# Kernel tuning notes

Measured on AMD Instinct MI355X. Metric: run time of the kernel, lower is better.

## Reference

```python
import jax, jax.numpy as jnp
import numpy as np

B, S, D = 2, 2048, 2048
H, DH, DC = 16, 128, 32  # heads, head dim, compressed dim


def setup_inputs() -> dict:
    key = jax.random.key(0)
    ks = jax.random.split(key, 9)
    sc = 0.02
    return {
        "hidden_states": jax.random.normal(ks[0], (B, S, D), jnp.float32),
        "Wq": jax.random.normal(ks[1], (D, D), jnp.float32) * sc,
        "Wk": jax.random.normal(ks[2], (D, D), jnp.float32) * sc,
        "Wv": jax.random.normal(ks[3], (D, D), jnp.float32) * sc,
        "Wo": jax.random.normal(ks[4], (D, D), jnp.float32) * sc,
        "Wkc": jax.random.normal(ks[5], (DH, DC), jnp.float32) * sc,
        "Wvc": jax.random.normal(ks[6], (DH, DC), jnp.float32) * sc,
        "Wke": jax.random.normal(ks[7], (DC, DH), jnp.float32) * sc,
        "Wve": jax.random.normal(ks[8], (DC, DH), jnp.float32) * sc,
    }


def reference(hidden_states, Wq, Wk, Wv, Wo, Wkc, Wvc, Wke, Wve):
    # Project to per-head Q/K/V: [B, H, S, DH]
    def proj(W):
        return jnp.einsum("bsd,de->bse", hidden_states, W).reshape(B, S, H, DH).transpose(0, 2, 1, 3)

    q = proj(Wq)
    k_full = proj(Wk)
    v_full = proj(Wv)

    # Compress K/V (low-rank down-projection, per head): [B, H, S, DC]
    k_compressed = jnp.einsum("bhsd,dc->bhsc", k_full, Wkc)
    v_compressed = jnp.einsum("bhsd,dc->bhsc", v_full, Wvc)

    # Expand compressed cache back to full head dim (expand_mode='pre')
    k_hat = jnp.einsum("bhsc,cd->bhsd", k_compressed, Wke)
    v_hat = jnp.einsum("bhsc,cd->bhsd", v_compressed, Wve)

    # Causal scaled-dot-product attention
    scale = 1.0 / jnp.sqrt(jnp.asarray(DH, jnp.float32))
    scores = jnp.einsum("bhqd,bhkd->bhqk", q, k_hat) * scale
    causal = jnp.tril(jnp.ones((S, S), bool))
    scores = jnp.where(causal[None, None], scores, jnp.finfo(scores.dtype).min)
    probs = jax.nn.softmax(scores, axis=-1)
    ctx = jnp.einsum("bhqk,bhkd->bhqd", probs, v_hat)  # [B, H, S, DH]

    attn_out = jnp.einsum("bsd,de->bse", ctx.transpose(0, 2, 1, 3).reshape(B, S, D), Wo)
    return attn_out, k_compressed, v_compressed
```

## Files before the change

### kernel.cpp

```cpp
#include <hip/hip_runtime.h>

using u16 = unsigned short;
using u32 = unsigned int;

typedef __attribute__((ext_vector_type(8))) __bf16 bf16x8;
typedef __attribute__((ext_vector_type(4))) float f32x4;
typedef __attribute__((ext_vector_type(4))) u32 u32x4;

#define GLOAD16(gp, lp) __builtin_amdgcn_global_load_lds( \
    (const __attribute__((address_space(1))) void*)(gp),  \
    (__attribute__((address_space(3))) void*)(lp), 16, 0, 0)

__device__ __forceinline__ u16 f2b(float f) {
  u32 u = __builtin_bit_cast(u32, f);
  u += 0x7fffu + ((u >> 16) & 1u);
  return (u16)(u >> 16);
}
__device__ __forceinline__ float b2f(u16 h) {
  return __builtin_bit_cast(float, (u32)h << 16);
}
__device__ __forceinline__ u32 cvtpk(float lo, float hi) {
  u32 r;
  asm("v_cvt_pk_bf16_f32 %0, %1, %2" : "=v"(r) : "v"(lo), "v"(hi));
  return r;
}

__global__ __launch_bounds__(256) void cast_k(
    const float* __restrict__ in, u16* __restrict__ o1, int n) {
  int i = (blockIdx.x * 256 + threadIdx.x) * 4;
  if (i >= n) return;
  float4 v = *(const float4*)&in[i];
  *(uint2*)&o1[i] = make_uint2((u32)f2b(v.x) | ((u32)f2b(v.y) << 16),
                               (u32)f2b(v.z) | ((u32)f2b(v.w) << 16));
}

__global__ __launch_bounds__(256) void transpose_cast_k(
    const float* __restrict__ in, u16* __restrict__ out, int D) {
  __shared__ float t[32][33];
  const int tx = threadIdx.x & 31, ty = threadIdx.x >> 5;
  const int e0 = blockIdx.x * 32, d0 = blockIdx.y * 32;
  #pragma unroll
  for (int i = ty; i < 32; i += 8) t[i][tx] = in[(size_t)(d0 + i) * D + e0 + tx];
  __syncthreads();
  #pragma unroll
  for (int i = ty; i < 32; i += 8) out[(size_t)(e0 + i) * D + d0 + tx] = f2b(t[tx][i]);
}

__global__ __launch_bounds__(256) void combine_k(
    const float* __restrict__ Wfull, const float* __restrict__ Wc,
    u16* __restrict__ outT, int D) {
  __shared__ float wl[4096];
  const int tid = threadIdx.x;
  for (int i = tid; i < 4096; i += 256) wl[i] = Wc[i];
  __syncthreads();
  const int h = blockIdx.y;
  const int d = blockIdx.x * 256 + tid;
  const float* wkr = Wfull + (size_t)d * D + h * 128;
  float acc[32] = {};
  for (int dp = 0; dp < 128; ++dp) {
    const float wv = wkr[dp];
    const float* w2 = &wl[dp * 32];
    #pragma unroll
    for (int c = 0; c < 32; ++c) acc[c] += wv * w2[c];
  }
  #pragma unroll
  for (int c = 0; c < 32; ++c)
    outT[(size_t)(h * 32 + c) * D + d] = f2b(acc[c]);
}

__global__ __launch_bounds__(256) void wtrans_k(
    const float* __restrict__ in, u16* __restrict__ out) {
  const int i = blockIdx.x * 256 + threadIdx.x;
  const int d = i >> 5, c = i & 31;
  out[i] = f2b(in[c * 128 + d]);
}

template <int TRANS>
__global__ __launch_bounds__(256) void expand_mfma_k(
    const u16* __restrict__ in, const u16* __restrict__ WT, u16* __restrict__ out) {
  __shared__ alignas(16) u16 WL[128 * 32];
  __shared__ alignas(16) u16 ct[64 * 40];
  const int tid = threadIdx.x, lane = tid & 63, w = tid >> 6;
  const int cl = lane & 15, g = lane >> 4;
  const int bh = blockIdx.y, s0 = blockIdx.x * 64;
  for (int i = tid; i < 512; i += 256) ((uint4*)WL)[i] = ((const uint4*)WT)[i];
  {
    const int r = tid >> 2, co = (tid & 3) * 8;
    *(uint4*)&ct[r * 40 + co] =
        *(const uint4*)&in[((size_t)bh * 2048 + s0 + r) * 32 + co];
  }
  __syncthreads();
  f32x4 acc[2][4] = {};
  #pragma unroll
  for (int dti = 0; dti < 2; ++dti) {
    const bf16x8 wf = *(const bf16x8*)&WL[((w * 2 + dti) * 16 + cl) * 32 + g * 8];
    #pragma unroll
    for (int st = 0; st < 4; ++st) {
      const bf16x8 cf = *(const bf16x8*)&ct[(st * 16 + cl) * 40 + g * 8];
      if constexpr (TRANS)
        acc[dti][st] = __builtin_amdgcn_mfma_f32_16x16x32_bf16(wf, cf, acc[dti][st], 0, 0, 0);
      else
        acc[dti][st] = __builtin_amdgcn_mfma_f32_16x16x32_bf16(cf, wf, acc[dti][st], 0, 0, 0);
    }
  }
  #pragma unroll
  for (int dti = 0; dti < 2; ++dti) {
    #pragma unroll
    for (int st = 0; st < 4; ++st) {
      #pragma unroll
      for (int r = 0; r < 4; ++r) {
        if constexpr (TRANS) {
          const int d = (w * 2 + dti) * 16 + g * 4 + r;
          const int s = s0 + st * 16 + cl;
          out[((size_t)bh * 128 + d) * 2048 + s] = f2b(acc[dti][st][r]);
        } else {
          const int s = s0 + st * 16 + g * 4 + r;
          const int d = (w * 2 + dti) * 16 + cl;
          out[((size_t)bh * 2048 + s) * 128 + d] = f2b(acc[dti][st][r]);
        }
      }
    }
  }
}

__global__ __launch_bounds__(256) void gemm_qkv_k(
    const u16* __restrict__ A, const u16* __restrict__ Bt,
    u16* __restrict__ qb, float* __restrict__ out_kc, u16* __restrict__ kcb,
    float* __restrict__ out_vc, u16* __restrict__ vcb) {
  __shared__ alignas(16) u16 As[128 * 64];
  __shared__ alignas(16) u16 Bs[128 * 64];
  const int tid = threadIdx.x, lane = tid & 63, w = tid >> 6;
  const int l15 = lane & 15, lhi = lane >> 4;
  const int m0 = blockIdx.y * 128, n0 = blockIdx.x * 128;
  const int wr = (w >> 1) * 64, wc = (w & 1) * 64;
  const int rl = lane >> 3, cbe = (lane & 7) * 8;
  const int K = 2048;

  f32x4 acc[4][4] = {};

  for (int k0 = 0; k0 < K; k0 += 64) {
    __syncthreads();
    #pragma unroll
    for (int i = 0; i < 4; ++i) {
      const int rb = w * 32 + i * 8;
      GLOAD16(A + (size_t)(m0 + rb + rl) * K + k0 + cbe, &As[rb * 64]);
      GLOAD16(Bt + (size_t)(n0 + rb + rl) * K + k0 + cbe, &Bs[rb * 64]);
    }
    __syncthreads();
    #pragma unroll
    for (int ks = 0; ks < 2; ++ks) {
      bf16x8 af[4], bfr[4];
      #pragma unroll
      for (int m = 0; m < 4; ++m)
        af[m] = *(const bf16x8*)&As[(wr + m * 16 + l15) * 64 + ks * 32 + lhi * 8];
      #pragma unroll
      for (int n = 0; n < 4; ++n)
        bfr[n] = *(const bf16x8*)&Bs[(wc + n * 16 + l15) * 64 + ks * 32 + lhi * 8];
      #pragma unroll
      for (int m = 0; m < 4; ++m)
        #pragma unroll
        for (int n = 0; n < 4; ++n)
          acc[m][n] = __builtin_amdgcn_mfma_f32_16x16x32_bf16(af[m], bfr[n], acc[m][n], 0, 0, 0);
    }
  }

  const float qscale = 0.08838834764831845f * 1.4426950408889634f;
  #pragma unroll
  for (int m = 0; m < 4; ++m) {
    #pragma unroll
    for (int n = 0; n < 4; ++n) {
      #pragma unroll
      for (int r = 0; r < 4; ++r) {
        const int row = m0 + wr + m * 16 + lhi * 4 + r;
        const int col = n0 + wc + n * 16 + l15;
        const int b = row >> 11, s = row & 2047;
        const float v = acc[m][n][r];
        if (n0 < 2048) {
          const int h = col >> 7, dh = col & 127;
          qb[((size_t)(b * 16 + h) * 2048 + s) * 128 + dh] = f2b(v * qscale);
        } else {
          const int cc = col - 2048;
          if (cc < 512) {
            const int h = cc >> 5, c = cc & 31;
            const size_t idx = ((size_t)(b * 16 + h) * 2048 + s) * 32 + c;
            out_kc[idx] = v;
            kcb[idx] = f2b(v);
          } else {
            const int cc2 = cc - 512;
            const int h = cc2 >> 5, c = cc2 & 31;
            const size_t idx = ((size_t)(b * 16 + h) * 2048 + s) * 32 + c;
            out_vc[idx] = v;
            vcb[idx] = f2b(v);
          }
        }
      }
    }
  }
}

__global__ __launch_bounds__(256) void gemm_o_k(
    const u16* __restrict__ A, const u16* __restrict__ Bt,
    int M, int N, int K, float* __restrict__ outF) {
  __shared__ alignas(16) u16 As[128 * 64];
  __shared__ alignas(16) u16 Bs[128 * 64];
  const int tid = threadIdx.x, lane = tid & 63, w = tid >> 6;
  const int l15 = lane & 15, lhi = lane >> 4;
  const int m0 = blockIdx.y * 128, n0 = blockIdx.x * 128;
  const int wr = (w >> 1) * 64, wc = (w & 1) * 64;
  const int rl = lane >> 3, cbe = (lane & 7) * 8;

  f32x4 acc[4][4] = {};

  for (int k0 = 0; k0 < K; k0 += 64) {
    __syncthreads();
    #pragma unroll
    for (int i = 0; i < 4; ++i) {
      const int rb = w * 32 + i * 8;
      GLOAD16(A + (size_t)(m0 + rb + rl) * K + k0 + cbe, &As[rb * 64]);
      GLOAD16(Bt + (size_t)(n0 + rb + rl) * K + k0 + cbe, &Bs[rb * 64]);
    }
    __syncthreads();
    #pragma unroll
    for (int ks = 0; ks < 2; ++ks) {
      bf16x8 af[4], bfr[4];
      #pragma unroll
      for (int m = 0; m < 4; ++m)
        af[m] = *(const bf16x8*)&As[(wr + m * 16 + l15) * 64 + ks * 32 + lhi * 8];
      #pragma unroll
      for (int n = 0; n < 4; ++n)
        bfr[n] = *(const bf16x8*)&Bs[(wc + n * 16 + l15) * 64 + ks * 32 + lhi * 8];
      #pragma unroll
      for (int m = 0; m < 4; ++m)
        #pragma unroll
        for (int n = 0; n < 4; ++n)
          acc[m][n] = __builtin_amdgcn_mfma_f32_16x16x32_bf16(af[m], bfr[n], acc[m][n], 0, 0, 0);
    }
  }

  #pragma unroll
  for (int m = 0; m < 4; ++m)
    #pragma unroll
    for (int n = 0; n < 4; ++n)
      #pragma unroll
      for (int r = 0; r < 4; ++r)
        outF[(size_t)(m0 + wr + m * 16 + lhi * 4 + r) * N + n0 + wc + n * 16 + l15] =
            acc[m][n][r];
}

__global__ __launch_bounds__(512, 4) void attn_k(
    const u16* __restrict__ q, const u16* __restrict__ kh,
    const u16* __restrict__ vt, u16* __restrict__ ctx) {
  __shared__ alignas(16) u16 Ks[2][64 * 128];
  __shared__ alignas(16) u16 Vs[2][128 * 64];
  const int tid = threadIdx.x, lane = tid & 63, w = tid >> 6;
  const int grp = w >> 2, wq = w & 3;
  const int c = lane & 15, g = lane >> 4;
  const int iA = blockIdx.x, iB = 31 - iA, bh = blockIdx.y;
  const int qt = grp ? iB : iA;
  const size_t base = (size_t)bh * (2048 * 128);

  bf16x8 qf[4];
  {
    const int qrow = qt * 64 + wq * 16 + c;
    #pragma unroll
    for (int ks = 0; ks < 4; ++ks)
      qf[ks] = *(const bf16x8*)&q[base + (size_t)qrow * 128 + ks * 32 + g * 8];
  }

  f32x4 of[8] = {};
  float m = -__builtin_inff(), l = 0.f;
  const int srcLo = lane ^ (((4 - g) & 3) << 4);
  const int srcHi = lane ^ (((g + 1) & 3) << 4);
  const int alS = (lane & 48) + ((lane & 48) >> 2);
  const bool hiSel = (g >> 1) != 0;

#define STAGE(J, BUF)                                                          \
  {                                                                            \
    _Pragma("unroll")                                                          \
    for (int i2 = 0; i2 < 2; ++i2) {                                           \
      const int rowgrp = w * 8 + i2 * 4;                                       \
      const int rloc = rowgrp + (lane >> 4);                                   \
      const int srce = ((c * 16) ^ ((rloc & 7) << 4)) >> 1;                    \
      GLOAD16(kh + base + (size_t)((J) * 64 + rloc) * 128 + srce,              \
              &Ks[BUF][rowgrp * 128]);                                         \
    }                                                                          \
    _Pragma("unroll")                                                          \
    for (int i2 = 0; i2 < 2; ++i2) {                                           \
      const int d0 = (w * 2 + i2) * 8;                                         \
      const int dd = d0 + (lane >> 3);                                         \
      const int cc = lane & 7;                                                 \
      GLOAD16(vt + base + (size_t)dd * 2048 + (J) * 64 + ((cc ^ (dd & 7)) * 8),\
              &Vs[BUF][d0 * 64]);                                              \
    }                                                                          \
  }

  STAGE(0, 0);
  for (int j = 0; j <= iB; ++j) {
    const int buf = j & 1;
    __syncthreads();
    if (j < iB) STAGE(j + 1, buf ^ 1);
    if (j <= qt) {
      f32x4 sf[4] = {};
      const char* ksb0 = (const char*)&Ks[buf][0];
      __builtin_amdgcn_s_setprio(1);
      #pragma unroll
      for (int n = 0; n < 4; ++n) {
        const int row = n * 16 + c;
        const char* kb = ksb0 + row * 256;
        #pragma unroll
        for (int ks = 0; ks < 4; ++ks) {
          const bf16x8 kf =
              *(const bf16x8*)(kb + ((ks * 64 + g * 16) ^ ((row & 7) << 4)));
          sf[n] = __builtin_amdgcn_mfma_f32_16x16x32_bf16(kf, qf[ks], sf[n], 0, 0, 0);
        }
      }
      __builtin_amdgcn_s_setprio(0);
      if (j == qt) {
        const int qloc = wq * 16 + c;
        #pragma unroll
        for (int n = 0; n < 4; ++n)
          #pragma unroll
          for (int r = 0; r < 4; ++r)
            if (n * 16 + g * 4 + r > qloc) sf[n][r] = -__builtin_inff();
      }
      float smax = sf[0][0];
      #pragma unroll
      for (int n = 0; n < 4; ++n)
        #pragma unroll
        for (int r = 0; r < 4; ++r) smax = fmaxf(smax, sf[n][r]);
      smax = fmaxf(smax, __shfl_xor(smax, 16, 64));
      smax = fmaxf(smax, __shfl_xor(smax, 32, 64));
      if (__any(smax - m > 12.0f)) {
        const float mn = fmaxf(m, smax);
        const float al = exp2f(m - mn);
        m = mn;
        l *= al;
        float alr[4];
        #pragma unroll
        for (int r = 0; r < 4; ++r) alr[r] = __shfl(al, alS + r, 64);
        #pragma unroll
        for (int nd = 0; nd < 8; ++nd)
          #pragma unroll
          for (int r = 0; r < 4; ++r) of[nd][r] *= alr[r];
      }
      float rs = 0.f;
      #pragma unroll
      for (int n = 0; n < 4; ++n)
        #pragma unroll
        for (int r = 0; r < 4; ++r) {
          const float p = exp2f(sf[n][r] - m);
          sf[n][r] = p;
          rs += p;
        }
      rs += __shfl_xor(rs, 16, 64);
      rs += __shfl_xor(rs, 32, 64);
      l += rs;
      u32 pk0[4], pk1[4];
      #pragma unroll
      for (int n = 0; n < 4; ++n) {
        pk0[n] = cvtpk(sf[n][0], sf[n][1]);
        pk1[n] = cvtpk(sf[n][2], sf[n][3]);
      }
      bf16x8 pf[2];
      #pragma unroll
      for (int ks2 = 0; ks2 < 2; ++ks2) {
        const int na = ks2 * 2, nb = ks2 * 2 + 1;
        const u32 a0 = (u32)__shfl((int)pk0[na], srcLo, 64);
        const u32 b0 = (u32)__shfl((int)pk0[nb], srcLo, 64);
        const u32 a1 = (u32)__shfl((int)pk1[na], srcLo, 64);
        const u32 b1 = (u32)__shfl((int)pk1[nb], srcLo, 64);
        const u32 a2 = (u32)__shfl((int)pk0[na], srcHi, 64);
        const u32 b2 = (u32)__shfl((int)pk0[nb], srcHi, 64);
        const u32 a3 = (u32)__shfl((int)pk1[na], srcHi, 64);
        const u32 b3 = (u32)__shfl((int)pk1[nb], srcHi, 64);
        const u32x4 wv = {hiSel ? b0 : a0, hiSel ? b1 : a1, hiSel ? b2 : a2,
                          hiSel ? b3 : a3};
        pf[ks2] = __builtin_bit_cast(bf16x8, wv);
      }
      const char* vsb0 = (const char*)&Vs[buf][0];
      __builtin_amdgcn_s_setprio(1);
      #pragma unroll
      for (int ks2 = 0; ks2 < 2; ++ks2) {
        #pragma unroll
        for (int nd = 0; nd < 8; ++nd) {
          const int row = nd * 16 + c;
          const bf16x8 vf = *(const bf16x8*)(vsb0 + row * 128 +
              ((ks2 * 64 + g * 16) ^ ((row & 7) << 4)));
          of[nd] = __builtin_amdgcn_mfma_f32_16x16x32_bf16(pf[ks2], vf, of[nd], 0, 0, 0);
        }
      }
      __builtin_amdgcn_s_setprio(0);
    }
  }

  const int bq = bh >> 4, hq = bh & 15;
  {
    float linv[4];
    #pragma unroll
    for (int r = 0; r < 4; ++r) linv[r] = 1.0f / __shfl(l, alS + r, 64);
    #pragma unroll
    for (int nd = 0; nd < 8; ++nd) {
      #pragma unroll
      for (int r = 0; r < 4; ++r) {
        const int row = qt * 64 + wq * 16 + g * 4 + r;
        ctx[((size_t)(bq * 2048 + row)) * 2048 + hq * 128 + nd * 16 + c] =
            f2b(of[nd][r] * linv[r]);
      }
    }
  }
#undef STAGE
}

extern "C" void kernel_launch(void* const* d_in, const int* in_sizes, int n_in,
                              void* d_out, int out_size, void* d_ws, size_t ws_size,
                              hipStream_t stream) {
  const float* hs  = (const float*)d_in[0];
  const float* Wq  = (const float*)d_in[1];
  const float* Wk  = (const float*)d_in[2];
  const float* Wv  = (const float*)d_in[3];
  const float* Wo  = (const float*)d_in[4];
  const float* Wkc = (const float*)d_in[5];
  const float* Wvc = (const float*)d_in[6];
  const float* Wke = (const float*)d_in[7];
  const float* Wve = (const float*)d_in[8];
  float* out      = (float*)d_out;
  float* out_attn = out;
  float* out_kc   = out + 8388608;
  float* out_vc   = out_kc + 2097152;

  char* ws = (char*)d_ws;
  u16* hsb   = (u16*)ws; ws += 16777216;
  u16* BtAll = (u16*)ws; ws += 12582912;
  u16* kcb   = (u16*)ws; ws += 4194304;
  u16* vcb   = (u16*)ws; ws += 4194304;
  u16* WoT   = (u16*)ws; ws += 8388608;
  u16* qb    = (u16*)ws; ws += 16777216;
  u16* vht   = (u16*)ws; ws += 16777216;
  u16* WkeT  = (u16*)ws; ws += 8192;
  u16* WveT  = (u16*)ws; ws += 8192;
  u16* khb   = hsb;
  u16* ctxb  = BtAll;

  cast_k<<<8192, 256, 0, stream>>>(hs, hsb, 8388608);
  transpose_cast_k<<<dim3(64, 64), 256, 0, stream>>>(Wq, BtAll, 2048);
  transpose_cast_k<<<dim3(64, 64), 256, 0, stream>>>(Wo, WoT, 2048);
  combine_k<<<dim3(8, 16), 256, 0, stream>>>(Wk, Wkc, BtAll + (size_t)2048 * 2048, 2048);
  combine_k<<<dim3(8, 16), 256, 0, stream>>>(Wv, Wvc, BtAll + (size_t)2560 * 2048, 2048);
  wtrans_k<<<16, 256, 0, stream>>>(Wke, WkeT);
  wtrans_k<<<16, 256, 0, stream>>>(Wve, WveT);

  gemm_qkv_k<<<dim3(24, 32), 256, 0, stream>>>(hsb, BtAll, qb, out_kc, kcb, out_vc, vcb);

  expand_mfma_k<0><<<dim3(32, 32), 256, 0, stream>>>(kcb, WkeT, khb);
  expand_mfma_k<1><<<dim3(32, 32), 256, 0, stream>>>(vcb, WveT, vht);

  attn_k<<<dim3(16, 32), 512, 0, stream>>>(qb, khb, vht, ctxb);

  gemm_o_k<<<dim3(16, 32), 256, 0, stream>>>(ctxb, WoT, 4096, 2048, 2048, out_attn);
}
```

Before: 442.9 us.

## Replace QKV and output GEMMs with a 4-stage ring-buffered 256-row tile kernel

Both projection GEMMs now use one templated kernel with 512 threads, 256xBN tiles and a four-deep LDS ring of K=32 slices. Each slice is prefetched three steps ahead with direct global-to-LDS loads, and explicit vmcnt waits plus a single barrier per step let memory latency overlap the MFMA work. It also sets MFMA priority and loosens attn_k launch bounds to 2 blocks per CU. The cost is more LDS and registers per block, one block per CU, and a grid of only 256 blocks, which may leave some CUs idle.

```diff
diff --git a/kernel.cpp b/kernel.cpp
--- a/kernel.cpp
+++ b/kernel.cpp
@@ -123,131 +123,117 @@
   }
 }
 
-__global__ __launch_bounds__(256) void gemm_qkv_k(
+template <int BN, int MODE>
+__global__ __launch_bounds__(512, 1) void gemm_ring_k(
     const u16* __restrict__ A, const u16* __restrict__ Bt,
     u16* __restrict__ qb, float* __restrict__ out_kc, u16* __restrict__ kcb,
-    float* __restrict__ out_vc, u16* __restrict__ vcb) {
-  __shared__ alignas(16) u16 As[128 * 64];
-  __shared__ alignas(16) u16 Bs[128 * 64];
+    float* __restrict__ out_vc, u16* __restrict__ vcb,
+    float* __restrict__ outF) {
+  constexpr int NR = BN / 64;
+  __shared__ alignas(16) u16 As[4][256 * 32];
+  __shared__ alignas(16) u16 Bs[4][BN * 32];
   const int tid = threadIdx.x, lane = tid & 63, w = tid >> 6;
   const int l15 = lane & 15, lhi = lane >> 4;
-  const int m0 = blockIdx.y * 128, n0 = blockIdx.x * 128;
-  const int wr = (w >> 1) * 64, wc = (w & 1) * 64;
-  const int rl = lane >> 3, cbe = (lane & 7) * 8;
-  const int K = 2048;
-
-  f32x4 acc[4][4] = {};
-
-  for (int k0 = 0; k0 < K; k0 += 64) {
-    __syncthreads();
-    #pragma unroll
-    for (int i = 0; i < 4; ++i) {
-      const int rb = w * 32 + i * 8;
-      GLOAD16(A + (size_t)(m0 + rb + rl) * K + k0 + cbe, &As[rb * 64]);
-      GLOAD16(Bt + (size_t)(n0 + rb + rl) * K + k0 + cbe, &Bs[rb * 64]);
-    }
-    __syncthreads();
-    #pragma unroll
-    for (int ks = 0; ks < 2; ++ks) {
-      bf16x8 af[4], bfr[4];
-      #pragma unroll
-      for (int m = 0; m < 4; ++m)
-        af[m] = *(const bf16x8*)&As[(wr + m * 16 + l15) * 64 + ks * 32 + lhi * 8];
-      #pragma unroll
-      for (int n = 0; n < 4; ++n)
-        bfr[n] = *(const bf16x8*)&Bs[(wc + n * 16 + l15) * 64 + ks * 32 + lhi * 8];
-      #pragma unroll
-      for (int m = 0; m < 4; ++m)
-        #pragma unroll
-        for (int n = 0; n < 4; ++n)
-          acc[m][n] = __builtin_amdgcn_mfma_f32_16x16x32_bf16(af[m], bfr[n], acc[m][n], 0, 0, 0);
-    }
-  }
+  const int m0 = blockIdx.y * 256, n0 = blockIdx.x * BN;
+  const int wr = (w >> 2) * 128, wc = (w & 3) * (BN / 4);
+
+  f32x4 acc[8][NR] = {};
+
+#define GSTAGE(T, BUF)                                                        \
+  {                                                                           \
+    const int kk0 = (T) * 32;                                                 \
+    const int idx0 = tid;                                                     \
+    GLOAD16(A + (size_t)(m0 + (idx0 >> 2)) * 2048 + kk0 + (idx0 & 3) * 8,     \
+            &As[BUF][idx0 * 8]);                                              \
+    const int idx1 = 512 + tid;                                               \
+    GLOAD16(A + (size_t)(m0 + (idx1 >> 2)) * 2048 + kk0 + (idx1 & 3) * 8,     \
+            &As[BUF][idx1 * 8]);                                              \
+    const int jdx0 = tid;                                                     \
+    GLOAD16(Bt + (size_t)(n0 + (jdx0 >> 2)) * 2048 + kk0 + (jdx0 & 3) * 8,    \
+            &Bs[BUF][jdx0 * 8]);                                              \
+    if constexpr (BN == 192) {                                                \
+      const int jdx1 = 512 + (tid & 255);   \
+      GLOAD16(Bt + (size_t)(n0 + (jdx1 >> 2)) * 2048 + kk0 + (jdx1 & 3) * 8,  \
+              &Bs[BUF][jdx1 * 8]);                                            \
+    }                                                                         \
+  }
+
+  GSTAGE(0, 0);
+  GSTAGE(1, 1);
+  GSTAGE(2, 2);
+
+  for (int t = 0; t < 64; ++t) {
+    const int buf = t & 3;
+    if (t < 62) {
+      if constexpr (BN == 192) asm volatile("s_waitcnt vmcnt(8)" ::: "memory");
+      else                     asm volatile("s_waitcnt vmcnt(6)" ::: "memory");
+    } else if (t == 62) {
+      if constexpr (BN == 192) asm volatile("s_waitcnt vmcnt(4)" ::: "memory");
+      else                     asm volatile("s_waitcnt vmcnt(3)" ::: "memory");
+    } else {
+      asm volatile("s_waitcnt vmcnt(0)" ::: "memory");
+    }
+    __builtin_amdgcn_s_barrier();
+    asm volatile("" ::: "memory");
+
+    bf16x8 bfrag[NR];
+    #pragma unroll
+    for (int n = 0; n < NR; ++n)
+      bfrag[n] = *(const bf16x8*)&Bs[buf][(wc + n * 16 + l15) * 32 + lhi * 8];
+    __builtin_amdgcn_s_setprio(1);
+    #pragma unroll
+    for (int m = 0; m < 8; ++m) {
+      const bf16x8 af = *(const bf16x8*)&As[buf][(wr + m * 16 + l15) * 32 + lhi * 8];
+      #pragma unroll
+      for (int n = 0; n < NR; ++n)
+        acc[m][n] = __builtin_amdgcn_mfma_f32_16x16x32_bf16(af, bfrag[n], acc[m][n], 0, 0, 0);
+    }
+    __builtin_amdgcn_s_setprio(0);
+    asm volatile("" ::: "memory");
+
+    if (t + 3 < 64) GSTAGE(t + 3, (t + 3) & 3);
+  }
+#undef GSTAGE
 
   const float qscale = 0.08838834764831845f * 1.4426950408889634f;
   #pragma unroll
-  for (int m = 0; m < 4; ++m) {
-    #pragma unroll
-    for (int n = 0; n < 4; ++n) {
+  for (int m = 0; m < 8; ++m) {
+    #pragma unroll
+    for (int n = 0; n < NR; ++n) {
       #pragma unroll
       for (int r = 0; r < 4; ++r) {
         const int row = m0 + wr + m * 16 + lhi * 4 + r;
         const int col = n0 + wc + n * 16 + l15;
-        const int b = row >> 11, s = row & 2047;
         const float v = acc[m][n][r];
-        if (n0 < 2048) {
-          const int h = col >> 7, dh = col & 127;
-          qb[((size_t)(b * 16 + h) * 2048 + s) * 128 + dh] = f2b(v * qscale);
+        if constexpr (MODE == 0) {
+          const int b = row >> 11, s = row & 2047;
+          if (col < 2048) {
+            const int h = col >> 7, dh = col & 127;
+            qb[((size_t)(b * 16 + h) * 2048 + s) * 128 + dh] = f2b(v * qscale);
+          } else {
+            const int cc = col - 2048;
+            if (cc < 512) {
+              const int h = cc >> 5, c = cc & 31;
+              const size_t idx = ((size_t)(b * 16 + h) * 2048 + s) * 32 + c;
+              out_kc[idx] = v;
+              kcb[idx] = f2b(v);
+            } else {
+              const int cc2 = cc - 512;
+              const int h = cc2 >> 5, c = cc2 & 31;
+              const size_t idx = ((size_t)(b * 16 + h) * 2048 + s) * 32 + c;
+              out_vc[idx] = v;
+              vcb[idx] = f2b(v);
+            }
+          }
         } else {
-          const int cc = col - 2048;
-          if (cc < 512) {
-            const int h = cc >> 5, c = cc & 31;
-            const size_t idx = ((size_t)(b * 16 + h) * 2048 + s) * 32 + c;
-            out_kc[idx] = v;
-            kcb[idx] = f2b(v);
-          } else {
-            const int cc2 = cc - 512;
-            const int h = cc2 >> 5, c = cc2 & 31;
-            const size_t idx = ((size_t)(b * 16 + h) * 2048 + s) * 32 + c;
-            out_vc[idx] = v;
-            vcb[idx] = f2b(v);
-          }
+          outF[(size_t)row * 2048 + col] = v;
         }
       }
     }
   }
 }
 
-__global__ __launch_bounds__(256) void gemm_o_k(
-    const u16* __restrict__ A, const u16* __restrict__ Bt,
-    int M, int N, int K, float* __restrict__ outF) {
-  __shared__ alignas(16) u16 As[128 * 64];
-  __shared__ alignas(16) u16 Bs[128 * 64];
-  const int tid = threadIdx.x, lane = tid & 63, w = tid >> 6;
-  const int l15 = lane & 15, lhi = lane >> 4;
-  const int m0 = blockIdx.y * 128, n0 = blockIdx.x * 128;
-  const int wr = (w >> 1) * 64, wc = (w & 1) * 64;
-  const int rl = lane >> 3, cbe = (lane & 7) * 8;
-
-  f32x4 acc[4][4] = {};
-
-  for (int k0 = 0; k0 < K; k0 += 64) {
-    __syncthreads();
-    #pragma unroll
-    for (int i = 0; i < 4; ++i) {
-      const int rb = w * 32 + i * 8;
-      GLOAD16(A + (size_t)(m0 + rb + rl) * K + k0 + cbe, &As[rb * 64]);
-      GLOAD16(Bt + (size_t)(n0 + rb + rl) * K + k0 + cbe, &Bs[rb * 64]);
-    }
-    __syncthreads();
-    #pragma unroll
-    for (int ks = 0; ks < 2; ++ks) {
-      bf16x8 af[4], bfr[4];
-      #pragma unroll
-      for (int m = 0; m < 4; ++m)
-        af[m] = *(const bf16x8*)&As[(wr + m * 16 + l15) * 64 + ks * 32 + lhi * 8];
-      #pragma unroll
-      for (int n = 0; n < 4; ++n)
-        bfr[n] = *(const bf16x8*)&Bs[(wc + n * 16 + l15) * 64 + ks * 32 + lhi * 8];
-      #pragma unroll
-      for (int m = 0; m < 4; ++m)
-        #pragma unroll
-        for (int n = 0; n < 4; ++n)
-          acc[m][n] = __builtin_amdgcn_mfma_f32_16x16x32_bf16(af[m], bfr[n], acc[m][n], 0, 0, 0);
-    }
-  }
-
-  #pragma unroll
-  for (int m = 0; m < 4; ++m)
-    #pragma unroll
-    for (int n = 0; n < 4; ++n)
-      #pragma unroll
-      for (int r = 0; r < 4; ++r)
-        outF[(size_t)(m0 + wr + m * 16 + lhi * 4 + r) * N + n0 + wc + n * 16 + l15] =
-            acc[m][n][r];
-}
-
-__global__ __launch_bounds__(512, 4) void attn_k(
+__global__ __launch_bounds__(512, 2) void attn_k(
     const u16* __restrict__ q, const u16* __restrict__ kh,
     const u16* __restrict__ vt, u16* __restrict__ ctx) {
   __shared__ alignas(16) u16 Ks[2][64 * 128];
@@ -449,12 +435,14 @@
   wtrans_k<<<16, 256, 0, stream>>>(Wke, WkeT);
   wtrans_k<<<16, 256, 0, stream>>>(Wve, WveT);
 
-  gemm_qkv_k<<<dim3(24, 32), 256, 0, stream>>>(hsb, BtAll, qb, out_kc, kcb, out_vc, vcb);
+  gemm_ring_k<192, 0><<<dim3(16, 16), 512, 0, stream>>>(
+      hsb, BtAll, qb, out_kc, kcb, out_vc, vcb, nullptr);
 
   expand_mfma_k<0><<<dim3(32, 32), 256, 0, stream>>>(kcb, WkeT, khb);
   expand_mfma_k<1><<<dim3(32, 32), 256, 0, stream>>>(vcb, WveT, vht);
 
   attn_k<<<dim3(16, 32), 512, 0, stream>>>(qb, khb, vht, ctxb);
 
-  gemm_o_k<<<dim3(16, 32), 256, 0, stream>>>(ctxb, WoT, 4096, 2048, 2048, out_attn);
-}
+  gemm_ring_k<128, 1><<<dim3(16, 16), 512, 0, stream>>>(
+      ctxb, WoT, nullptr, nullptr, nullptr, nullptr, nullptr, out_attn);
+}
```

New measurement: 448.0 us. Within noise of the previous version (+1.2%).
